# Kernel optimization log

Measured on AMD Instinct MI355X. Metric: run time of the kernel, lower is better.

## Reference

```python
import jax, jax.numpy as jnp
import numpy as np

HIDDEN = 768
NUM_LABELS = 25


def setup_inputs() -> dict:
    key = jax.random.key(0)
    k1, k2, k3, k4, k5 = jax.random.split(key, 5)
    B, H, S, E = 2, 12, 256, 64
    attention_probs = jax.random.uniform(k1, (B, H, S, S), dtype=jnp.float32)
    value_attentions = jax.random.normal(k2, (B, H, S, E), dtype=jnp.float32)
    relative_positions = jax.random.normal(k3, (B, S, S, H * E), dtype=jnp.float32)
    # nn.Linear(hidden_size, num_labels): weight [L, hidden], bias [L]
    bound = 1.0 / np.sqrt(HIDDEN)
    W = jax.random.uniform(k4, (NUM_LABELS, HIDDEN), dtype=jnp.float32, minval=-bound, maxval=bound)
    b = jax.random.uniform(k5, (NUM_LABELS,), dtype=jnp.float32, minval=-bound, maxval=bound)
    return {
        "attention_probs": attention_probs,
        "value_attentions": value_attentions,
        "relative_positions": relative_positions,
        "W": W,
        "b": b,
    }


def reference(attention_probs, value_attentions, relative_positions, W, b):
    B, H, S, E = value_attentions.shape
    # out[b,h,i,j,e] = probs[b,h,i,j] * (value[b,h,j,e] + rel[b,h,i,j,e])
    p = attention_probs[..., None]                      # [B,H,S,S,1]
    v = value_attentions[:, :, None, :, :]              # [B,H,1,S,E] broadcast over i
    rel = relative_positions.reshape(B, S, S, H, E).transpose(0, 3, 1, 2, 4)  # [B,H,S,S,E]
    out = p * (v + rel)                                 # [B,H,i,j,E]
    # permute(0,3,2,1,4) -> [B, j, i, H, E] -> [B,S,S,H*E]
    out = out.transpose(0, 3, 2, 1, 4).reshape(B, S, S, H * E)
    out = out @ W.T + b                                 # [B,S,S,L]
    return out.transpose(0, 1, 3, 2)                    # [B,S,L,S]
```

## Files before the change

kernel.cpp:

```cpp
#include <hip/hip_runtime.h>
#include <hip/hip_bf16.h>

#define NB 2
#define NH 12
#define NS 256
#define NE 64
#define NC 768
#define NL 25

#define CH 128
#define NCH 6
#define TI 128
#define SAS 132

typedef __attribute__((ext_vector_type(8))) short short8;
typedef __attribute__((ext_vector_type(4))) float float4v;

__device__ __forceinline__ unsigned short bfb(float x) {
    __hip_bfloat16 h = __float2bfloat16(x);
    return *reinterpret_cast<unsigned short*>(&h);
}
__device__ __forceinline__ unsigned int pk2(float x, float y) {
    return (unsigned int)bfb(x) | ((unsigned int)bfb(y) << 16);
}

__global__ void prep_w(const float* __restrict__ W, unsigned short* __restrict__ Wb) {
    int idx = blockIdx.x * 256 + threadIdx.x;
    if (idx >= 32 * NC) return;
    int row = idx / NC;
    int col = idx - row * NC;
    Wb[idx] = (row < NL) ? bfb(W[row * NC + col]) : (unsigned short)0;
}

__global__ __launch_bounds__(256, 4) void tmhs_mfma(
    const float* __restrict__ p,
    const float* __restrict__ v,
    const float* __restrict__ rel,
    const unsigned short* __restrict__ Wb,
    const float* __restrict__ bias,
    float* __restrict__ out)
{
    __shared__ unsigned short sA[TI][SAS];

    const int tid = threadIdx.x;
    const int bx  = blockIdx.x;
    const int ih  = bx & 1;
    const int j   = (bx >> 1) & 255;
    const int b   = bx >> 9;
    const int i0  = ih * TI;

    const int lane = tid & 63;
    const int wv   = tid >> 6;
    const int n15  = lane & 15;
    const int quad = lane >> 4;

    float4v z = {0.f, 0.f, 0.f, 0.f};
    float4v acc[2][2] = {{z, z}, {z, z}};

    const int srow  = tid >> 1;
    const int shalf = tid & 1;

    for (int ch = 0; ch < NCH; ++ch) {
        const int kc = ch * CH;
        const int h  = (kc >> 6) + shalf;
        __syncthreads();
        {
            const float  pr = p[((b*NH + h)*NS + (i0 + srow))*NS + j];
            const float4* rs = (const float4*)(rel + ((b*NS + i0 + srow)*NS + j)*NC + kc + shalf*64);
            const float4* vs = (const float4*)(v + ((b*NH + h)*NS + j)*NE);
            unsigned int* dst = (unsigned int*)&sA[srow][shalf*64];
#pragma unroll
            for (int q = 0; q < 16; ++q) {
                const float4 rr = rs[q];
                const float4 vv = vs[q];
                uint2 w2;
                w2.x = pk2(pr*(rr.x+vv.x), pr*(rr.y+vv.y));
                w2.y = pk2(pr*(rr.z+vv.z), pr*(rr.w+vv.w));
                *(uint2*)(dst + q*2) = w2;
            }
        }
        __syncthreads();

#pragma unroll
        for (int ks = 0; ks < 4; ++ks) {
            short8 af0 = *(const short8*)(Wb + (     n15)*NC + kc + ks*32 + quad*8);
            short8 af1 = *(const short8*)(Wb + (16 + n15)*NC + kc + ks*32 + quad*8);
#pragma unroll
            for (int nt = 0; nt < 2; ++nt) {
                const unsigned short* bp = &sA[wv*32 + nt*16 + n15][ks*32 + quad*8];
                union { short8 s8; unsigned long long d[2]; } bu;
                bu.d[0] = *(const unsigned long long*)bp;
                bu.d[1] = *(const unsigned long long*)(bp + 4);
                acc[0][nt] = __builtin_amdgcn_mfma_f32_16x16x32_bf16(af0, bu.s8, acc[0][nt], 0, 0, 0);
                acc[1][nt] = __builtin_amdgcn_mfma_f32_16x16x32_bf16(af1, bu.s8, acc[1][nt], 0, 0, 0);
            }
        }
    }

    const int obase = ((b*NS + j)*NL)*NS;
#pragma unroll
    for (int nt = 0; nt < 2; ++nt) {
        const int ii = i0 + wv*32 + nt*16 + n15;
#pragma unroll
        for (int mt = 0; mt < 2; ++mt) {
#pragma unroll
            for (int r = 0; r < 4; ++r) {
                const int l = mt*16 + quad*4 + r;
                if (l < NL)
                    out[obase + l*NS + ii] = acc[mt][nt][r] + bias[l];
            }
        }
    }
}

extern "C" void kernel_launch(void* const* d_in, const int* in_sizes, int n_in,
                              void* d_out, int out_size, void* d_ws, size_t ws_size,
                              hipStream_t stream) {
    const float* p    = (const float*)d_in[0];
    const float* v    = (const float*)d_in[1];
    const float* rel  = (const float*)d_in[2];
    const float* W    = (const float*)d_in[3];
    const float* bias = (const float*)d_in[4];
    float* out = (float*)d_out;
    unsigned short* Wb = (unsigned short*)d_ws;

    prep_w<<<dim3((32*NC + 255)/256), dim3(256), 0, stream>>>(W, Wb);
    tmhs_mfma<<<dim3(NB * NS * 2), dim3(256), 0, stream>>>(p, v, rel, Wb, bias, out);
}
```

Baseline: 560.8 us.

## Load rel directly into MFMA B-fragments, dropping LDS staging and per-chunk barriers

Each lane now reads its own rel rows straight from global memory in MFMA fragment layout, applies p*(rel+v) in registers, and converts to bf16 for the MFMA. The shared-memory staging of the bf16 A tile and the two barriers per chunk go away. p and v for the block are staged once in LDS up front. The cost is global loads where each lane reads 32 contiguous bytes from a different row, which may coalesce worse than the previous row-contiguous loads.

Result: no change. 563.9 us (+0.5%).

```diff
diff --git a/kernel.cpp b/kernel.cpp
--- a/kernel.cpp
+++ b/kernel.cpp
@@ -7,11 +7,7 @@
 #define NE 64
 #define NC 768
 #define NL 25
-
-#define CH 128
-#define NCH 6
 #define TI 128
-#define SAS 132
 
 typedef __attribute__((ext_vector_type(8))) short short8;
 typedef __attribute__((ext_vector_type(4))) float float4v;
@@ -19,9 +15,6 @@
 __device__ __forceinline__ unsigned short bfb(float x) {
     __hip_bfloat16 h = __float2bfloat16(x);
     return *reinterpret_cast<unsigned short*>(&h);
-}
-__device__ __forceinline__ unsigned int pk2(float x, float y) {
-    return (unsigned int)bfb(x) | ((unsigned int)bfb(y) << 16);
 }
 
 __global__ void prep_w(const float* __restrict__ W, unsigned short* __restrict__ Wb) {
@@ -40,7 +33,8 @@
     const float* __restrict__ bias,
     float* __restrict__ out)
 {
-    __shared__ unsigned short sA[TI][SAS];
+    __shared__ float sP[NH * TI];
+    __shared__ float sV[NC];
 
     const int tid = threadIdx.x;
     const int bx  = blockIdx.x;
@@ -48,6 +42,16 @@
     const int j   = (bx >> 1) & 255;
     const int b   = bx >> 9;
     const int i0  = ih * TI;
+
+    for (int t = tid; t < NH * TI; t += 256) {
+        const int h = t >> 7, i = t & 127;
+        sP[t] = p[((b*NH + h)*NS + i0 + i)*NS + j];
+    }
+    for (int t = tid; t < NC; t += 256) {
+        const int h = t >> 6, e = t & 63;
+        sV[t] = v[((b*NH + h)*NS + j)*NE + e];
+    }
+    __syncthreads();
 
     const int lane = tid & 63;
     const int wv   = tid >> 6;
@@ -57,44 +61,42 @@
     float4v z = {0.f, 0.f, 0.f, 0.f};
     float4v acc[2][2] = {{z, z}, {z, z}};
 
-    const int srow  = tid >> 1;
-    const int shalf = tid & 1;
+    const int iA = wv*32 + n15;
+    const int iB = iA + 16;
+    const float* relA = rel + ((b*NS + i0 + iA)*NS + j) * NC;
+    const float* relB = rel + ((b*NS + i0 + iB)*NS + j) * NC;
+    const unsigned short* w0 = Wb + n15 * NC;
+    const unsigned short* w1 = Wb + (16 + n15) * NC;
 
-    for (int ch = 0; ch < NCH; ++ch) {
-        const int kc = ch * CH;
-        const int h  = (kc >> 6) + shalf;
-        __syncthreads();
-        {
-            const float  pr = p[((b*NH + h)*NS + (i0 + srow))*NS + j];
-            const float4* rs = (const float4*)(rel + ((b*NS + i0 + srow)*NS + j)*NC + kc + shalf*64);
-            const float4* vs = (const float4*)(v + ((b*NH + h)*NS + j)*NE);
-            unsigned int* dst = (unsigned int*)&sA[srow][shalf*64];
-#pragma unroll
-            for (int q = 0; q < 16; ++q) {
-                const float4 rr = rs[q];
-                const float4 vv = vs[q];
-                uint2 w2;
-                w2.x = pk2(pr*(rr.x+vv.x), pr*(rr.y+vv.y));
-                w2.y = pk2(pr*(rr.z+vv.z), pr*(rr.w+vv.w));
-                *(uint2*)(dst + q*2) = w2;
-            }
-        }
-        __syncthreads();
+#pragma unroll 2
+    for (int ks = 0; ks < 24; ++ks) {
+        const int c0 = ks*32 + quad*8;
+        const float4 a0 = *(const float4*)(relA + c0);
+        const float4 a1 = *(const float4*)(relA + c0 + 4);
+        const float4 b0 = *(const float4*)(relB + c0);
+        const float4 b1 = *(const float4*)(relB + c0 + 4);
+        const short8 af0 = *(const short8*)(w0 + c0);
+        const short8 af1 = *(const short8*)(w1 + c0);
+        const float4 v0 = *(const float4*)(sV + c0);
+        const float4 v1 = *(const float4*)(sV + c0 + 4);
+        const int   h  = c0 >> 6;
+        const float pA = sP[h*TI + iA];
+        const float pB = sP[h*TI + iB];
 
-#pragma unroll
-        for (int ks = 0; ks < 4; ++ks) {
-            short8 af0 = *(const short8*)(Wb + (     n15)*NC + kc + ks*32 + quad*8);
-            short8 af1 = *(const short8*)(Wb + (16 + n15)*NC + kc + ks*32 + quad*8);
-#pragma unroll
-            for (int nt = 0; nt < 2; ++nt) {
-                const unsigned short* bp = &sA[wv*32 + nt*16 + n15][ks*32 + quad*8];
-                union { short8 s8; unsigned long long d[2]; } bu;
-                bu.d[0] = *(const unsigned long long*)bp;
-                bu.d[1] = *(const unsigned long long*)(bp + 4);
-                acc[0][nt] = __builtin_amdgcn_mfma_f32_16x16x32_bf16(af0, bu.s8, acc[0][nt], 0, 0, 0);
-                acc[1][nt] = __builtin_amdgcn_mfma_f32_16x16x32_bf16(af1, bu.s8, acc[1][nt], 0, 0, 0);
-            }
-        }
+        union { short8 s; unsigned short u[8]; } fa, fb;
+        fa.u[0] = bfb(pA*(a0.x+v0.x)); fa.u[1] = bfb(pA*(a0.y+v0.y));
+        fa.u[2] = bfb(pA*(a0.z+v0.z)); fa.u[3] = bfb(pA*(a0.w+v0.w));
+        fa.u[4] = bfb(pA*(a1.x+v1.x)); fa.u[5] = bfb(pA*(a1.y+v1.y));
+        fa.u[6] = bfb(pA*(a1.z+v1.z)); fa.u[7] = bfb(pA*(a1.w+v1.w));
+        fb.u[0] = bfb(pB*(b0.x+v0.x)); fb.u[1] = bfb(pB*(b0.y+v0.y));
+        fb.u[2] = bfb(pB*(b0.z+v0.z)); fb.u[3] = bfb(pB*(b0.w+v0.w));
+        fb.u[4] = bfb(pB*(b1.x+v1.x)); fb.u[5] = bfb(pB*(b1.y+v1.y));
+        fb.u[6] = bfb(pB*(b1.z+v1.z)); fb.u[7] = bfb(pB*(b1.w+v1.w));
+
+        acc[0][0] = __builtin_amdgcn_mfma_f32_16x16x32_bf16(af0, fa.s, acc[0][0], 0, 0, 0);
+        acc[1][0] = __builtin_amdgcn_mfma_f32_16x16x32_bf16(af1, fa.s, acc[1][0], 0, 0, 0);
+        acc[0][1] = __builtin_amdgcn_mfma_f32_16x16x32_bf16(af0, fb.s, acc[0][1], 0, 0, 0);
+        acc[1][1] = __builtin_amdgcn_mfma_f32_16x16x32_bf16(af1, fb.s, acc[1][1], 0, 0, 0);
     }
 
     const int obase = ((b*NS + j)*NL)*NS;
```
